# Performance work log

Measured on AMD Instinct MI355X. Metric: run time of the kernel, lower is better.

The kernel has to match this reference:

```python
import jax, jax.numpy as jnp
import numpy as np

B, DIN, D, T, C = 32768, 784, 256, 16, 64


def setup_inputs() -> dict:
    key = jax.random.key(0)
    ks = jax.random.split(key, 4)
    x = jax.random.normal(ks[0], (B, DIN), dtype=jnp.float32)
    Wp = jax.random.normal(ks[1], (DIN, D), dtype=jnp.float32) / np.sqrt(DIN).astype(np.float32)
    bp = jnp.zeros((D,), jnp.float32)
    sigs_raw = jax.random.normal(ks[2], (T, D), dtype=jnp.float32) * 0.5
    Wc = jax.random.normal(ks[3], (T, D, C), dtype=jnp.float32) / np.sqrt(D).astype(np.float32)
    bc = jnp.zeros((T, C), jnp.float32)
    return {"x": x, "Wp": Wp, "bp": bp, "sigs_raw": sigs_raw, "Wc": Wc, "bc": bc}


def _quantize_ternary(s):
    # straight-through ternary quantization with +/-0.3 thresholds
    q = jnp.where(s > 0.3, 1.0, jnp.where(s < -0.3, -1.0, 0.0)).astype(s.dtype)
    return s + jax.lax.stop_gradient(q - s)


def reference(x, Wp, bp, sigs_raw, Wc, bc):
    h = x @ Wp + bp                                   # [B, D]
    sigs = _quantize_ternary(sigs_raw)                # [T, D] ternary signatures
    scores = h @ sigs.T                               # [B, T]
    tile_indices = jnp.argmax(scores, axis=-1)        # [B] top-1 routing
    # per-tile linear classifiers, then select the routed tile's logits
    all_logits = jnp.einsum('bd,tdc->btc', h, Wc) + bc[None]   # [B, T, C]
    logits = jnp.take_along_axis(all_logits, tile_indices[:, None, None], axis=1)[:, 0, :]
    return logits, tile_indices
```

## Files before the change

### kernel.cpp

```cpp
#include <hip/hip_runtime.h>

typedef short short8 __attribute__((ext_vector_type(8)));
typedef float f32x4 __attribute__((ext_vector_type(4)));

#define B_ROWS 32768
#define DIN 784
#define D_DIM 256
#define T_TILES 16
#define C_DIM 64
#define BM 64
#define NCHUNK 25

#define WPT_OFF    0u
#define WCT_OFF    409600u
#define WS_OFF     933888u
#define BS_OFF     1036288u
#define H_OFF      1036416u
#define BUCKET_OFF 17813632u
#define CNT_OFF    19910784u

static __device__ inline unsigned short f2bf(float f) {
    unsigned u = __builtin_bit_cast(unsigned, f);
    u += 0x7fffu + ((u >> 16) & 1u);
    return (unsigned short)(u >> 16);
}
static __device__ inline double qtern(float s) {
    double v = (double)s;
    return (v > 0.3) ? 1.0 : ((v < -0.3) ? -1.0 : 0.0);
}

__global__ __launch_bounds__(256)
void prep_kernel(const float* __restrict__ Wp, const float* __restrict__ bp,
                 const float* __restrict__ sigs_raw, const float* __restrict__ Wc,
                 char* __restrict__ ws) {
    __shared__ __align__(16) char u2[34816];
    const int bid = blockIdx.x, tid = threadIdx.x;
    unsigned short* wpt = (unsigned short*)(ws + WPT_OFF);
    unsigned short* wct = (unsigned short*)(ws + WCT_OFF);
    double* Wsd = (double*)(ws + WS_OFF);
    double* bsd = (double*)(ws + BS_OFF);

    if (bid < 25) {
        unsigned short (*lt)[40] = (unsigned short (*)[40])u2;
        const int k0 = bid * 32;
        #pragma unroll
        for (int p = 0; p < 8; ++p) {
            const int k = p * 4 + (tid >> 6);
            const int c = (tid & 63) * 4;
            float4 v = make_float4(0.f, 0.f, 0.f, 0.f);
            if (k0 + k < DIN) v = *(const float4*)&Wp[(size_t)(k0 + k) * D_DIM + c];
            lt[c + 0][k] = f2bf(v.x); lt[c + 1][k] = f2bf(v.y);
            lt[c + 2][k] = f2bf(v.z); lt[c + 3][k] = f2bf(v.w);
        }
        __syncthreads();
        const float4* src = (const float4*)&lt[tid][0];
        float4* dst = (float4*)(wpt + bid * 8192 + tid * 32);
        dst[0] = src[0]; dst[1] = src[1]; dst[2] = src[2]; dst[3] = src[3];
    } else if (bid < 123) {
        float* sigq = (float*)u2;
        float* wp8  = (float*)(u2 + 16384);
        const int k0 = (bid - 25) * 8;
        #pragma unroll
        for (int i = 0; i < 16; ++i) {
            const int idx = i * 256 + tid;
            sigq[idx] = (float)qtern(sigs_raw[idx]);
        }
        #pragma unroll
        for (int i = 0; i < 8; ++i)
            wp8[i * 256 + tid] = Wp[(size_t)(k0 + i) * D_DIM + tid];
        __syncthreads();
        const int kk = tid >> 5, t = (tid >> 1) & 15, half = tid & 1;
        double s = 0.0;
        const float* wr = &wp8[kk * 256 + half * 128];
        const float* sq = &sigq[t * 256 + half * 128];
        for (int d = 0; d < 128; ++d) s += (double)wr[d] * (double)sq[d];
        s += __shfl_xor(s, 1);
        if (half == 0) Wsd[(k0 + kk) * 16 + t] = s;
    } else if (bid < 139) {
        unsigned short (*lc)[264] = (unsigned short (*)[264])u2;
        const int t = bid - 123;
        #pragma unroll
        for (int j = 0; j < 16; ++j) {
            const int f4 = j * 256 + tid;
            const int d  = f4 >> 4;
            const int c4 = (f4 & 15) * 4;
            const float4 v = *(const float4*)&Wc[((size_t)t * D_DIM + d) * C_DIM + c4];
            lc[c4 + 0][d] = f2bf(v.x); lc[c4 + 1][d] = f2bf(v.y);
            lc[c4 + 2][d] = f2bf(v.z); lc[c4 + 3][d] = f2bf(v.w);
        }
        __syncthreads();
        const int c = tid >> 2, d0 = (tid & 3) * 64;
        const float4* src = (const float4*)&lc[c][d0];
        float4* dst = (float4*)(wct + t * 16384 + c * 256 + d0);
        #pragma unroll
        for (int i = 0; i < 8; ++i) dst[i] = src[i];
    } else {
        int* cnt = (int*)(ws + CNT_OFF);
        if (tid < 16) cnt[tid] = 0;
        Wsd[12544 + tid] = 0.0;
        const int t = tid >> 4, l = tid & 15;
        double s = 0.0;
        #pragma unroll
        for (int j = 0; j < 16; ++j) {
            const int d = l * 16 + j;
            s += (double)bp[d] * qtern(sigs_raw[t * D_DIM + d]);
        }
        #pragma unroll
        for (int m = 8; m >= 1; m >>= 1) s += __shfl_xor(s, m);
        if (l == 0) bsd[t] = s;
    }
}

__global__ __launch_bounds__(256, 3)
void gemm_score_kernel(const float* __restrict__ x, const float* __restrict__ bp,
                       char* __restrict__ ws, float* __restrict__ out) {
    __shared__ __align__(16) char u[33792];
    __shared__ int tidx_s[BM];

    unsigned short* Abuf = (unsigned short*)u;
    char* wssb = u + 10240;

    const unsigned short* wpt = (const unsigned short*)(ws + WPT_OFF);
    unsigned short* hbf = (unsigned short*)(ws + H_OFF);
    const double* Wsd = (const double*)(ws + WS_OFF);
    const double* bsd = (const double*)(ws + BS_OFF);
    int* bucket = (int*)(ws + BUCKET_OFF);
    int* cnt = (int*)(ws + CNT_OFF);

    const int tid = threadIdx.x;
    const int row0 = blockIdx.x * BM;
    const int wid = tid >> 6, lane = tid & 63;
    const int wr = wid >> 1, wcid = wid & 1;
    const int lrow = lane & 15, kb8 = (lane >> 4) * 8;
    const int ar = tid >> 2, aq = tid & 3, ako = aq * 8;
    const int wtp = tid >> 5, wkk = tid & 31;

    f32x4 acc[2][8];
    #pragma unroll
    for (int i = 0; i < 2; ++i)
        #pragma unroll
        for (int j = 0; j < 8; ++j) acc[i][j] = (f32x4){0.f, 0.f, 0.f, 0.f};
    double accd[16];
    #pragma unroll
    for (int t = 0; t < 16; ++t) accd[t] = 0.0;
    float xs8[8];

    const int wsoff = wtp * 576 + wkk * 16 + (wkk >> 3) * 16;
    const char* wrd_base = wssb + aq * 144;

    {
        const float4* p = (const float4*)&x[(size_t)(row0 + ar) * DIN + ako];
        const float4 a0 = p[0], a1 = p[1];
        xs8[0] = a0.x; xs8[1] = a0.y; xs8[2] = a0.z; xs8[3] = a0.w;
        xs8[4] = a1.x; xs8[5] = a1.y; xs8[6] = a1.z; xs8[7] = a1.w;
        unsigned short tmp[8];
        #pragma unroll
        for (int i = 0; i < 8; ++i) tmp[i] = f2bf(xs8[i]);
        *(short8*)(Abuf + ar * 40 + ako) = *(short8*)tmp;
        const double2 wv = *(const double2*)&Wsd[wkk * 16 + wtp * 2];
        *(double2*)(wssb + wsoff) = wv;
    }
    __syncthreads();

    for (int c = 0; c < NCHUNK; ++c) {
        const int cur = c & 1;
        const bool more = (c + 1 < NCHUNK);

        short8 bfr[8];
        #pragma unroll
        for (int cf = 0; cf < 8; ++cf)
            bfr[cf] = *(const short8*)(wpt + c * 8192 + (wcid * 128 + cf * 16 + lrow) * 32 + kb8);

        float4 va0, va1; double2 wv;
        if (more) {
            const int kbase = (c + 1) * 32 + ako;
            if (kbase < DIN) {
                const float4* p = (const float4*)&x[(size_t)(row0 + ar) * DIN + kbase];
                va0 = p[0]; va1 = p[1];
            } else {
                va0 = make_float4(0, 0, 0, 0); va1 = make_float4(0, 0, 0, 0);
            }
            wv = *(const double2*)&Wsd[((c + 1) * 32 + wkk) * 16 + wtp * 2];
        }

        {
            const char* wb = wrd_base + cur * 4608;
            #pragma unroll
            for (int i = 0; i < 8; ++i) {
                const double xd = (double)xs8[i];
                #pragma unroll
                for (int tp = 0; tp < 8; ++tp) {
                    const double2 w2 = *(const double2*)(wb + tp * 576 + i * 16);
                    accd[2 * tp]     += xd * w2.x;
                    accd[2 * tp + 1] += xd * w2.y;
                }
            }
        }

        {
            const unsigned short* Ab = Abuf + cur * 2560;
            const short8 af0 = *(const short8*)(Ab + (wr * 32 + lrow) * 40 + kb8);
            const short8 af1 = *(const short8*)(Ab + (wr * 32 + 16 + lrow) * 40 + kb8);
            #pragma unroll
            for (int cf = 0; cf < 8; ++cf) {
                acc[0][cf] = __builtin_amdgcn_mfma_f32_16x16x32_bf16(af0, bfr[cf], acc[0][cf], 0, 0, 0);
                acc[1][cf] = __builtin_amdgcn_mfma_f32_16x16x32_bf16(af1, bfr[cf], acc[1][cf], 0, 0, 0);
            }
        }

        if (more) {
            xs8[0] = va0.x; xs8[1] = va0.y; xs8[2] = va0.z; xs8[3] = va0.w;
            xs8[4] = va1.x; xs8[5] = va1.y; xs8[6] = va1.z; xs8[7] = va1.w;
            unsigned short tmp[8];
            #pragma unroll
            for (int i = 0; i < 8; ++i) tmp[i] = f2bf(xs8[i]);
            *(short8*)(Abuf + (cur ^ 1) * 2560 + ar * 40 + ako) = *(short8*)tmp;
            *(double2*)(wssb + (cur ^ 1) * 4608 + wsoff) = wv;
        }
        __syncthreads();
    }

    unsigned short* h_s = (unsigned short*)u;
    #pragma unroll
    for (int cf = 0; cf < 8; ++cf) {
        const int gc = wcid * 128 + cf * 16 + lrow;
        const float bpv = bp[gc];
        #pragma unroll
        for (int rf = 0; rf < 2; ++rf) {
            const int lr = wr * 32 + rf * 16 + (lane >> 4) * 4;
            #pragma unroll
            for (int r = 0; r < 4; ++r)
                h_s[(lr + r) * 264 + gc] = f2bf(acc[rf][cf][r] + bpv);
        }
    }

    #pragma unroll
    for (int t = 0; t < 16; ++t) {
        accd[t] += __shfl_xor(accd[t], 1);
        accd[t] += __shfl_xor(accd[t], 2);
    }
    if (aq == 0) {
        double best = -1.0e300; int bi = 0;
        #pragma unroll
        for (int t = 0; t < 16; ++t) {
            const double v = accd[t] + bsd[t];
            if (v > best) { best = v; bi = t; }
        }
        tidx_s[ar] = bi;
        out[(size_t)B_ROWS * C_DIM + row0 + ar] = (float)bi;
    }
    __syncthreads();

    {
        const int r = tid >> 2, q = tid & 3;
        const float4* src = (const float4*)(h_s + r * 264 + q * 64);
        float4 v[8];
        #pragma unroll
        for (int i = 0; i < 8; ++i) v[i] = src[i];
        float4* dst = (float4*)(hbf + (size_t)(row0 + r) * D_DIM + q * 64);
        #pragma unroll
        for (int i = 0; i < 8; ++i) dst[i] = v[i];
    }

    if (tid < T_TILES) {
        int c = 0;
        for (int r = 0; r < BM; ++r) c += (tidx_s[r] == tid);
        int pos = atomicAdd(&cnt[tid], c);
        for (int r = 0; r < BM; ++r)
            if (tidx_s[r] == tid) bucket[tid * B_ROWS + (pos++)] = row0 + r;
    }
}

#define LBM 64
__global__ __launch_bounds__(256)
void logits_kernel(const float* __restrict__ bc, const char* __restrict__ ws,
                   float* __restrict__ out) {
    __shared__ __align__(16) unsigned short As[LBM * 136];
    __shared__ __align__(16) unsigned short Bs[64 * 136];
    __shared__ int rows_s[LBM];

    const int tid = threadIdx.x;
    const int t = blockIdx.x >> 9;
    const int c0 = (blockIdx.x & 511) * LBM;
    const int* cnt = (const int*)(ws + CNT_OFF);
    const int cntv = cnt[t];
    if (c0 >= cntv) return;

    const int* bucket = (const int*)(ws + BUCKET_OFF);
    const unsigned short* hbf = (const unsigned short*)(ws + H_OFF);
    const unsigned short* wct = (const unsigned short*)(ws + WCT_OFF);

    if (tid < LBM) {
        int i = c0 + tid; if (i >= cntv) i = cntv - 1;
        rows_s[tid] = bucket[t * B_ROWS + i];
    }
    __syncthreads();

    const int wid = tid >> 6, lane = tid & 63;
    const int wr = wid >> 1, wcid = wid & 1;
    const int lrow = lane & 15, kb8 = (lane >> 4) * 8;
    const int sr = tid >> 2, sq = tid & 3;

    f32x4 acc[2][2];
    #pragma unroll
    for (int i = 0; i < 2; ++i) { acc[i][0] = (f32x4){0,0,0,0}; acc[i][1] = (f32x4){0,0,0,0}; }

    #pragma unroll
    for (int ch = 0; ch < 2; ++ch) {
        const int k0 = ch * 128;
        if (ch) __syncthreads();
        {
            const float4* p = (const float4*)(hbf + (size_t)rows_s[sr] * D_DIM + k0 + sq * 32);
            float4 v[4];
            #pragma unroll
            for (int i = 0; i < 4; ++i) v[i] = p[i];
            float4* d = (float4*)(As + sr * 136 + sq * 32);
            #pragma unroll
            for (int i = 0; i < 4; ++i) d[i] = v[i];
        }
        {
            const float4* p = (const float4*)(wct + (size_t)t * 16384 + sr * 256 + k0 + sq * 32);
            float4 v[4];
            #pragma unroll
            for (int i = 0; i < 4; ++i) v[i] = p[i];
            float4* d = (float4*)(Bs + sr * 136 + sq * 32);
            #pragma unroll
            for (int i = 0; i < 4; ++i) d[i] = v[i];
        }
        __syncthreads();
        #pragma unroll
        for (int ks = 0; ks < 4; ++ks) {
            const int kb = ks * 32 + kb8;
            const short8 bf0 = *(const short8*)(Bs + (wcid * 32 + lrow) * 136 + kb);
            const short8 bf1 = *(const short8*)(Bs + (wcid * 32 + 16 + lrow) * 136 + kb);
            #pragma unroll
            for (int rf = 0; rf < 2; ++rf) {
                const short8 af = *(const short8*)(As + (wr * 32 + rf * 16 + lrow) * 136 + kb);
                acc[rf][0] = __builtin_amdgcn_mfma_f32_16x16x32_bf16(af, bf0, acc[rf][0], 0, 0, 0);
                acc[rf][1] = __builtin_amdgcn_mfma_f32_16x16x32_bf16(af, bf1, acc[rf][1], 0, 0, 0);
            }
        }
    }

    #pragma unroll
    for (int cf = 0; cf < 2; ++cf) {
        const int col = wcid * 32 + cf * 16 + lrow;
        const float bcv = bc[t * C_DIM + col];
        #pragma unroll
        for (int rf = 0; rf < 2; ++rf) {
            const int lr = wr * 32 + rf * 16 + (lane >> 4) * 4;
            #pragma unroll
            for (int r = 0; r < 4; ++r)
                out[(size_t)rows_s[lr + r] * C_DIM + col] = acc[rf][cf][r] + bcv;
        }
    }
}

extern "C" void kernel_launch(void* const* d_in, const int* in_sizes, int n_in,
                              void* d_out, int out_size, void* d_ws, size_t ws_size,
                              hipStream_t stream) {
    const float* x    = (const float*)d_in[0];
    const float* Wp   = (const float*)d_in[1];
    const float* bp   = (const float*)d_in[2];
    const float* sigs = (const float*)d_in[3];
    const float* Wc   = (const float*)d_in[4];
    const float* bc   = (const float*)d_in[5];
    float* out = (float*)d_out;
    char* ws = (char*)d_ws;

    prep_kernel<<<dim3(140), dim3(256), 0, stream>>>(Wp, bp, sigs, Wc, ws);
    gemm_score_kernel<<<dim3(B_ROWS / BM), dim3(256), 0, stream>>>(x, bp, ws, out);
    logits_kernel<<<dim3(16 * 512), dim3(256), 0, stream>>>(bc, ws, out);
}
```

Measured before the change: 239.1 us.

## Fuse projection, routing and per-tile logits into one kernel with in-block bucketing

```diff
diff --git a/kernel.cpp b/kernel.cpp
--- a/kernel.cpp
+++ b/kernel.cpp
@@ -1,6 +1,7 @@
 #include <hip/hip_runtime.h>
 
 typedef short short8 __attribute__((ext_vector_type(8)));
+typedef short short4v __attribute__((ext_vector_type(4)));
 typedef float f32x4 __attribute__((ext_vector_type(4)));
 
 #define B_ROWS 32768
@@ -9,15 +10,13 @@
 #define T_TILES 16
 #define C_DIM 64
 #define BM 64
+#define NT 512
 #define NCHUNK 25
 
-#define WPT_OFF    0u
-#define WCT_OFF    409600u
-#define WS_OFF     933888u
-#define BS_OFF     1036288u
-#define H_OFF      1036416u
-#define BUCKET_OFF 17813632u
-#define CNT_OFF    19910784u
+#define WPT_OFF 0u
+#define WCT_OFF 409600u
+#define WS_OFF  933888u
+#define BS_OFF  1036288u
 
 static __device__ inline unsigned short f2bf(float f) {
     unsigned u = __builtin_bit_cast(unsigned, f);
@@ -37,7 +36,7 @@
     const int bid = blockIdx.x, tid = threadIdx.x;
     unsigned short* wpt = (unsigned short*)(ws + WPT_OFF);
     unsigned short* wct = (unsigned short*)(ws + WCT_OFF);
-    double* Wsd = (double*)(ws + WS_OFF);
+    double* Ws2 = (double*)(ws + WS_OFF);
     double* bsd = (double*)(ws + BS_OFF);
 
     if (bid < 25) {
@@ -53,9 +52,13 @@
             lt[c + 2][k] = f2bf(v.z); lt[c + 3][k] = f2bf(v.w);
         }
         __syncthreads();
-        const float4* src = (const float4*)&lt[tid][0];
-        float4* dst = (float4*)(wpt + bid * 8192 + tid * 32);
-        dst[0] = src[0]; dst[1] = src[1]; dst[2] = src[2]; dst[3] = src[3];
+        #pragma unroll
+        for (int i = 0; i < 4; ++i) {
+            const int f = i * 256 + tid;
+            const int g = f >> 6, l = f & 63;
+            const short8 v = *(const short8*)&lt[g * 16 + (l & 15)][(l >> 4) * 8];
+            *(short8*)(wpt + (size_t)bid * 8192 + f * 8) = v;
+        }
     } else if (bid < 123) {
         float* sigq = (float*)u2;
         float* wp8  = (float*)(u2 + 16384);
@@ -75,7 +78,7 @@
         const float* sq = &sigq[t * 256 + half * 128];
         for (int d = 0; d < 128; ++d) s += (double)wr[d] * (double)sq[d];
         s += __shfl_xor(s, 1);
-        if (half == 0) Wsd[(k0 + kk) * 16 + t] = s;
+        if (half == 0) Ws2[(size_t)t * 800 + k0 + kk] = s;
     } else if (bid < 139) {
         unsigned short (*lc)[264] = (unsigned short (*)[264])u2;
         const int t = bid - 123;
@@ -89,15 +92,16 @@
             lc[c4 + 2][d] = f2bf(v.z); lc[c4 + 3][d] = f2bf(v.w);
         }
         __syncthreads();
-        const int c = tid >> 2, d0 = (tid & 3) * 64;
-        const float4* src = (const float4*)&lc[c][d0];
-        float4* dst = (float4*)(wct + t * 16384 + c * 256 + d0);
-        #pragma unroll
-        for (int i = 0; i < 8; ++i) dst[i] = src[i];
+        #pragma unroll
+        for (int i = 0; i < 8; ++i) {
+            const int f = i * 256 + tid;
+            const int l = f & 63, cfks = f >> 6;
+            const int cf = cfks & 3, ks = cfks >> 2;
+            const short8 v = *(const short8*)&lc[cf * 16 + (l & 15)][ks * 32 + (l >> 4) * 8];
+            *(short8*)(wct + (size_t)t * 16384 + f * 8) = v;
+        }
     } else {
-        int* cnt = (int*)(ws + CNT_OFF);
-        if (tid < 16) cnt[tid] = 0;
-        Wsd[12544 + tid] = 0.0;
+        Ws2[(size_t)(tid >> 4) * 800 + 784 + (tid & 15)] = 0.0;
         const int t = tid >> 4, l = tid & 15;
         double s = 0.0;
         #pragma unroll
@@ -111,119 +115,101 @@
     }
 }
 
-__global__ __launch_bounds__(256, 3)
-void gemm_score_kernel(const float* __restrict__ x, const float* __restrict__ bp,
-                       char* __restrict__ ws, float* __restrict__ out) {
+__global__ __launch_bounds__(NT, 4)
+void fused_kernel(const float* __restrict__ x, const float* __restrict__ bp,
+                  const float* __restrict__ bc, const char* __restrict__ ws,
+                  float* __restrict__ out) {
     __shared__ __align__(16) char u[33792];
+    __shared__ __align__(16) double score_s[64 * 17];
     __shared__ int tidx_s[BM];
-
-    unsigned short* Abuf = (unsigned short*)u;
-    char* wssb = u + 10240;
+    __shared__ int counts_s[16], starts_s[17];
+    __shared__ int rows_local[BM];
+    __shared__ int sub_t[24], sub_s[24], sub_c[24], nsubs_s;
+
+    float*          xls  = (float*)u;
+    unsigned short* Abuf = (unsigned short*)(u + 16896);
 
     const unsigned short* wpt = (const unsigned short*)(ws + WPT_OFF);
-    unsigned short* hbf = (unsigned short*)(ws + H_OFF);
-    const double* Wsd = (const double*)(ws + WS_OFF);
+    const unsigned short* wct = (const unsigned short*)(ws + WCT_OFF);
+    const double* Wsg = (const double*)(ws + WS_OFF);
     const double* bsd = (const double*)(ws + BS_OFF);
-    int* bucket = (int*)(ws + BUCKET_OFF);
-    int* cnt = (int*)(ws + CNT_OFF);
-
-    const int tid = threadIdx.x;
+
+    const int tid  = threadIdx.x;
     const int row0 = blockIdx.x * BM;
-    const int wid = tid >> 6, lane = tid & 63;
-    const int wr = wid >> 1, wcid = wid & 1;
-    const int lrow = lane & 15, kb8 = (lane >> 4) * 8;
-    const int ar = tid >> 2, aq = tid & 3, ako = aq * 8;
-    const int wtp = tid >> 5, wkk = tid & 31;
-
-    f32x4 acc[2][8];
+    const int wid  = tid >> 6, lane = tid & 63;
+    const int wr   = wid >> 2, wcid = wid & 3;
+    const int lrow = lane & 15, kgo = (lane >> 4) * 8;
+    const int ar   = tid >> 3, ako = (tid & 7) * 4;
+
+    const int wid_u = __builtin_amdgcn_readfirstlane(wid);
+    const double* W0 = Wsg + (size_t)(2 * wid_u) * 800;
+    const double* W1 = W0 + 800;
+
+    f32x4 acc[2][4];
     #pragma unroll
     for (int i = 0; i < 2; ++i)
         #pragma unroll
-        for (int j = 0; j < 8; ++j) acc[i][j] = (f32x4){0.f, 0.f, 0.f, 0.f};
-    double accd[16];
-    #pragma unroll
-    for (int t = 0; t < 16; ++t) accd[t] = 0.0;
-    float xs8[8];
-
-    const int wsoff = wtp * 576 + wkk * 16 + (wkk >> 3) * 16;
-    const char* wrd_base = wssb + aq * 144;
+        for (int j = 0; j < 4; ++j) acc[i][j] = (f32x4){0.f, 0.f, 0.f, 0.f};
+    double s0a = 0.0, s0b = 0.0, s1a = 0.0, s1b = 0.0;
 
     {
-        const float4* p = (const float4*)&x[(size_t)(row0 + ar) * DIN + ako];
-        const float4 a0 = p[0], a1 = p[1];
-        xs8[0] = a0.x; xs8[1] = a0.y; xs8[2] = a0.z; xs8[3] = a0.w;
-        xs8[4] = a1.x; xs8[5] = a1.y; xs8[6] = a1.z; xs8[7] = a1.w;
-        unsigned short tmp[8];
-        #pragma unroll
-        for (int i = 0; i < 8; ++i) tmp[i] = f2bf(xs8[i]);
-        *(short8*)(Abuf + ar * 40 + ako) = *(short8*)tmp;
-        const double2 wv = *(const double2*)&Wsd[wkk * 16 + wtp * 2];
-        *(double2*)(wssb + wsoff) = wv;
+        const float4 v = *(const float4*)&x[(size_t)(row0 + ar) * DIN + ako];
+        *(float4*)(xls + ar * 33 + ako) = v;
+        unsigned short t4[4] = {f2bf(v.x), f2bf(v.y), f2bf(v.z), f2bf(v.w)};
+        *(short4v*)(Abuf + ar * 40 + ako) = *(short4v*)t4;
     }
     __syncthreads();
 
     for (int c = 0; c < NCHUNK; ++c) {
         const int cur = c & 1;
         const bool more = (c + 1 < NCHUNK);
-
-        short8 bfr[8];
-        #pragma unroll
-        for (int cf = 0; cf < 8; ++cf)
-            bfr[cf] = *(const short8*)(wpt + c * 8192 + (wcid * 128 + cf * 16 + lrow) * 32 + kb8);
-
-        float4 va0, va1; double2 wv;
+        float4 vnx = make_float4(0.f, 0.f, 0.f, 0.f);
         if (more) {
-            const int kbase = (c + 1) * 32 + ako;
-            if (kbase < DIN) {
-                const float4* p = (const float4*)&x[(size_t)(row0 + ar) * DIN + kbase];
-                va0 = p[0]; va1 = p[1];
-            } else {
-                va0 = make_float4(0, 0, 0, 0); va1 = make_float4(0, 0, 0, 0);
-            }
-            wv = *(const double2*)&Wsd[((c + 1) * 32 + wkk) * 16 + wtp * 2];
-        }
-
-        {
-            const char* wb = wrd_base + cur * 4608;
-            #pragma unroll
-            for (int i = 0; i < 8; ++i) {
-                const double xd = (double)xs8[i];
-                #pragma unroll
-                for (int tp = 0; tp < 8; ++tp) {
-                    const double2 w2 = *(const double2*)(wb + tp * 576 + i * 16);
-                    accd[2 * tp]     += xd * w2.x;
-                    accd[2 * tp + 1] += xd * w2.y;
-                }
-            }
+            const int kb = (c + 1) * 32 + ako;
+            if (kb < DIN) vnx = *(const float4*)&x[(size_t)(row0 + ar) * DIN + kb];
         }
 
         {
             const unsigned short* Ab = Abuf + cur * 2560;
-            const short8 af0 = *(const short8*)(Ab + (wr * 32 + lrow) * 40 + kb8);
-            const short8 af1 = *(const short8*)(Ab + (wr * 32 + 16 + lrow) * 40 + kb8);
-            #pragma unroll
-            for (int cf = 0; cf < 8; ++cf) {
-                acc[0][cf] = __builtin_amdgcn_mfma_f32_16x16x32_bf16(af0, bfr[cf], acc[0][cf], 0, 0, 0);
-                acc[1][cf] = __builtin_amdgcn_mfma_f32_16x16x32_bf16(af1, bfr[cf], acc[1][cf], 0, 0, 0);
+            const short8 af0 = *(const short8*)(Ab + (wr * 32 + lrow) * 40 + kgo);
+            const short8 af1 = *(const short8*)(Ab + (wr * 32 + 16 + lrow) * 40 + kgo);
+            #pragma unroll
+            for (int cf = 0; cf < 4; ++cf) {
+                const int g = wcid * 4 + cf;
+                const short8 bfr = *(const short8*)(wpt + ((size_t)c * 16 + g) * 512 + lane * 8);
+                acc[0][cf] = __builtin_amdgcn_mfma_f32_16x16x32_bf16(af0, bfr, acc[0][cf], 0, 0, 0);
+                acc[1][cf] = __builtin_amdgcn_mfma_f32_16x16x32_bf16(af1, bfr, acc[1][cf], 0, 0, 0);
             }
         }
 
+        {
+            const float*  xr  = xls + cur * 2112 + lane * 33;
+            const double* W0c = W0 + c * 32;
+            const double* W1c = W1 + c * 32;
+            #pragma unroll
+            for (int j = 0; j < 8; ++j) {
+                const f32x4 xv = *(const f32x4*)(xr + j * 4);
+                const double x0 = (double)xv[0], x1 = (double)xv[1];
+                const double x2 = (double)xv[2], x3 = (double)xv[3];
+                s0a += x0 * W0c[j * 4 + 0]; s0b += x1 * W0c[j * 4 + 1];
+                s0a += x2 * W0c[j * 4 + 2]; s0b += x3 * W0c[j * 4 + 3];
+                s1a += x0 * W1c[j * 4 + 0]; s1b += x1 * W1c[j * 4 + 1];
+                s1a += x2 * W1c[j * 4 + 2]; s1b += x3 * W1c[j * 4 + 3];
+            }
+        }
+
         if (more) {
-            xs8[0] = va0.x; xs8[1] = va0.y; xs8[2] = va0.z; xs8[3] = va0.w;
-            xs8[4] = va1.x; xs8[5] = va1.y; xs8[6] = va1.z; xs8[7] = va1.w;
-            unsigned short tmp[8];
-            #pragma unroll
-            for (int i = 0; i < 8; ++i) tmp[i] = f2bf(xs8[i]);
-            *(short8*)(Abuf + (cur ^ 1) * 2560 + ar * 40 + ako) = *(short8*)tmp;
-            *(double2*)(wssb + (cur ^ 1) * 4608 + wsoff) = wv;
+            *(float4*)(xls + (cur ^ 1) * 2112 + ar * 33 + ako) = vnx;
+            unsigned short t4[4] = {f2bf(vnx.x), f2bf(vnx.y), f2bf(vnx.z), f2bf(vnx.w)};
+            *(short4v*)(Abuf + (cur ^ 1) * 2560 + ar * 40 + ako) = *(short4v*)t4;
         }
         __syncthreads();
     }
 
     unsigned short* h_s = (unsigned short*)u;
     #pragma unroll
-    for (int cf = 0; cf < 8; ++cf) {
-        const int gc = wcid * 128 + cf * 16 + lrow;
+    for (int cf = 0; cf < 4; ++cf) {
+        const int gc = wcid * 64 + cf * 16 + lrow;
         const float bpv = bp[gc];
         #pragma unroll
         for (int rf = 0; rf < 2; ++rf) {
@@ -233,125 +219,72 @@
                 h_s[(lr + r) * 264 + gc] = f2bf(acc[rf][cf][r] + bpv);
         }
     }
-
-    #pragma unroll
-    for (int t = 0; t < 16; ++t) {
-        accd[t] += __shfl_xor(accd[t], 1);
-        accd[t] += __shfl_xor(accd[t], 2);
-    }
-    if (aq == 0) {
-        double best = -1.0e300; int bi = 0;
-        #pragma unroll
-        for (int t = 0; t < 16; ++t) {
-            const double v = accd[t] + bsd[t];
-            if (v > best) { best = v; bi = t; }
-        }
-        tidx_s[ar] = bi;
-        out[(size_t)B_ROWS * C_DIM + row0 + ar] = (float)bi;
-    }
-    __syncthreads();
-
-    {
-        const int r = tid >> 2, q = tid & 3;
-        const float4* src = (const float4*)(h_s + r * 264 + q * 64);
-        float4 v[8];
-        #pragma unroll
-        for (int i = 0; i < 8; ++i) v[i] = src[i];
-        float4* dst = (float4*)(hbf + (size_t)(row0 + r) * D_DIM + q * 64);
-        #pragma unroll
-        for (int i = 0; i < 8; ++i) dst[i] = v[i];
-    }
-
-    if (tid < T_TILES) {
+    score_s[lane * 17 + 2 * wid]     = s0a + s0b + bsd[2 * wid];
+    score_s[lane * 17 + 2 * wid + 1] = s1a + s1b + bsd[2 * wid + 1];
+    __syncthreads();
+
+    if (tid < BM) {
+        const double* s = &score_s[tid * 17];
+        double best = s[0]; int bi = 0;
+        #pragma unroll
+        for (int t = 1; t < 16; ++t)
+            if (s[t] > best) { best = s[t]; bi = t; }
+        tidx_s[tid] = bi;
+        out[(size_t)B_ROWS * C_DIM + row0 + tid] = (float)bi;
+    }
+    __syncthreads();
+
+    if (tid < 16) {
         int c = 0;
         for (int r = 0; r < BM; ++r) c += (tidx_s[r] == tid);
-        int pos = atomicAdd(&cnt[tid], c);
+        counts_s[tid] = c;
+    }
+    __syncthreads();
+    if (tid == 0) {
+        int a = 0, n = 0;
+        for (int t = 0; t < 16; ++t) {
+            starts_s[t] = a;
+            int cc = counts_s[t], s = a;
+            a += cc;
+            while (cc > 0) { sub_t[n] = t; sub_s[n] = s; sub_c[n] = (cc < 16 ? cc : 16); s += 16; cc -= 16; ++n; }
+        }
+        starts_s[16] = a;
+        nsubs_s = n;
+    }
+    __syncthreads();
+    if (tid < 16) {
+        int pos = starts_s[tid];
         for (int r = 0; r < BM; ++r)
-            if (tidx_s[r] == tid) bucket[tid * B_ROWS + (pos++)] = row0 + r;
-    }
-}
-
-#define LBM 64
-__global__ __launch_bounds__(256)
-void logits_kernel(const float* __restrict__ bc, const char* __restrict__ ws,
-                   float* __restrict__ out) {
-    __shared__ __align__(16) unsigned short As[LBM * 136];
-    __shared__ __align__(16) unsigned short Bs[64 * 136];
-    __shared__ int rows_s[LBM];
-
-    const int tid = threadIdx.x;
-    const int t = blockIdx.x >> 9;
-    const int c0 = (blockIdx.x & 511) * LBM;
-    const int* cnt = (const int*)(ws + CNT_OFF);
-    const int cntv = cnt[t];
-    if (c0 >= cntv) return;
-
-    const int* bucket = (const int*)(ws + BUCKET_OFF);
-    const unsigned short* hbf = (const unsigned short*)(ws + H_OFF);
-    const unsigned short* wct = (const unsigned short*)(ws + WCT_OFF);
-
-    if (tid < LBM) {
-        int i = c0 + tid; if (i >= cntv) i = cntv - 1;
-        rows_s[tid] = bucket[t * B_ROWS + i];
-    }
-    __syncthreads();
-
-    const int wid = tid >> 6, lane = tid & 63;
-    const int wr = wid >> 1, wcid = wid & 1;
-    const int lrow = lane & 15, kb8 = (lane >> 4) * 8;
-    const int sr = tid >> 2, sq = tid & 3;
-
-    f32x4 acc[2][2];
-    #pragma unroll
-    for (int i = 0; i < 2; ++i) { acc[i][0] = (f32x4){0,0,0,0}; acc[i][1] = (f32x4){0,0,0,0}; }
-
-    #pragma unroll
-    for (int ch = 0; ch < 2; ++ch) {
-        const int k0 = ch * 128;
-        if (ch) __syncthreads();
-        {
-            const float4* p = (const float4*)(hbf + (size_t)rows_s[sr] * D_DIM + k0 + sq * 32);
-            float4 v[4];
-            #pragma unroll
-            for (int i = 0; i < 4; ++i) v[i] = p[i];
-            float4* d = (float4*)(As + sr * 136 + sq * 32);
-            #pragma unroll
-            for (int i = 0; i < 4; ++i) d[i] = v[i];
-        }
-        {
-            const float4* p = (const float4*)(wct + (size_t)t * 16384 + sr * 256 + k0 + sq * 32);
-            float4 v[4];
-            #pragma unroll
-            for (int i = 0; i < 4; ++i) v[i] = p[i];
-            float4* d = (float4*)(Bs + sr * 136 + sq * 32);
-            #pragma unroll
-            for (int i = 0; i < 4; ++i) d[i] = v[i];
-        }
-        __syncthreads();
-        #pragma unroll
-        for (int ks = 0; ks < 4; ++ks) {
-            const int kb = ks * 32 + kb8;
-            const short8 bf0 = *(const short8*)(Bs + (wcid * 32 + lrow) * 136 + kb);
-            const short8 bf1 = *(const short8*)(Bs + (wcid * 32 + 16 + lrow) * 136 + kb);
-            #pragma unroll
-            for (int rf = 0; rf < 2; ++rf) {
-                const short8 af = *(const short8*)(As + (wr * 32 + rf * 16 + lrow) * 136 + kb);
-                acc[rf][0] = __builtin_amdgcn_mfma_f32_16x16x32_bf16(af, bf0, acc[rf][0], 0, 0, 0);
-                acc[rf][1] = __builtin_amdgcn_mfma_f32_16x16x32_bf16(af, bf1, acc[rf][1], 0, 0, 0);
+            if (tidx_s[r] == tid) rows_local[pos++] = r;
+    }
+    __syncthreads();
+
+    const int ns = nsubs_s;
+    for (int si = wid; si < ns; si += 8) {
+        const int t = sub_t[si], sbase = sub_s[si], cnt = sub_c[si];
+        const int arow = rows_local[sbase + (lrow < cnt ? lrow : cnt - 1)];
+        f32x4 a2[4];
+        #pragma unroll
+        for (int i = 0; i < 4; ++i) a2[i] = (f32x4){0.f, 0.f, 0.f, 0.f};
+        #pragma unroll
+        for (int ks = 0; ks < 8; ++ks) {
+            const short8 af = *(const short8*)(h_s + arow * 264 + ks * 32 + kgo);
+            #pragma unroll
+            for (int cf = 0; cf < 4; ++cf) {
+                const short8 bf = *(const short8*)(wct + (size_t)t * 16384 + ((ks * 4 + cf) * 64 + lane) * 8);
+                a2[cf] = __builtin_amdgcn_mfma_f32_16x16x32_bf16(af, bf, a2[cf], 0, 0, 0);
             }
         }
-    }
-
-    #pragma unroll
-    for (int cf = 0; cf < 2; ++cf) {
-        const int col = wcid * 32 + cf * 16 + lrow;
-        const float bcv = bc[t * C_DIM + col];
-        #pragma unroll
-        for (int rf = 0; rf < 2; ++rf) {
-            const int lr = wr * 32 + rf * 16 + (lane >> 4) * 4;
-            #pragma unroll
-            for (int r = 0; r < 4; ++r)
-                out[(size_t)rows_s[lr + r] * C_DIM + col] = acc[rf][cf][r] + bcv;
+        #pragma unroll
+        for (int cf = 0; cf < 4; ++cf) {
+            const int col = cf * 16 + lrow;
+            const float bcv = bc[t * C_DIM + col];
+            #pragma unroll
+            for (int r = 0; r < 4; ++r) {
+                const int j = (lane >> 4) * 4 + r;
+                if (j < cnt)
+                    out[(size_t)(row0 + rows_local[sbase + j]) * C_DIM + col] = a2[cf][r] + bcv;
+            }
         }
     }
 }
@@ -369,6 +302,5 @@
     char* ws = (char*)d_ws;
 
     prep_kernel<<<dim3(140), dim3(256), 0, stream>>>(Wp, bp, sigs, Wc, ws);
-    gemm_score_kernel<<<dim3(B_ROWS / BM), dim3(256), 0, stream>>>(x, bp, ws, out);
-    logits_kernel<<<dim3(16 * 512), dim3(256), 0, stream>>>(bc, ws, out);
-}
+    fused_kernel<<<dim3(B_ROWS / BM), dim3(NT), 0, stream>>>(x, bp, bc, ws, out);
+}
```

Result: slower. 284.6 us (+19.0%).
